# Kernel tuning notes

Hardware: AMD Instinct MI355X
Metric: run time of the kernel (lower is better)

## Reference

```python
import jax, jax.numpy as jnp
import numpy as np

N, C, H, W = 8, 256, 56, 56
DEPTH, HEADS, NWIN, TOPK, MLPR = 4, 8, 7, 4, 4
EPS = 1e-6


def setup_inputs() -> dict:
    key = jax.random.key(0)
    ks = jax.random.split(key, 16)
    s = 0.02
    return {
        'x': jax.random.normal(ks[0], (N, C, H, W), jnp.float32),
        'ln1_w': jnp.ones((DEPTH, C), jnp.float32),
        'ln1_b': jnp.zeros((DEPTH, C), jnp.float32),
        'qkv_w': jax.random.normal(ks[1], (DEPTH, C, 3 * C), jnp.float32) * s,
        'qkv_b': jnp.zeros((DEPTH, 3 * C), jnp.float32),
        'lepe_w': jax.random.normal(ks[2], (DEPTH, C, 1, 5, 5), jnp.float32) * s,
        'lepe_b': jnp.zeros((DEPTH, C), jnp.float32),
        'wo_w': jax.random.normal(ks[3], (DEPTH, C, C), jnp.float32) * s,
        'wo_b': jnp.zeros((DEPTH, C), jnp.float32),
        'ln2_w': jnp.ones((DEPTH, C), jnp.float32),
        'ln2_b': jnp.zeros((DEPTH, C), jnp.float32),
        'mlp1_w': jax.random.normal(ks[4], (DEPTH, C, MLPR * C), jnp.float32) * s,
        'mlp1_b': jnp.zeros((DEPTH, MLPR * C), jnp.float32),
        'mlp2_w': jax.random.normal(ks[5], (DEPTH, MLPR * C, C), jnp.float32) * s,
        'mlp2_b': jnp.zeros((DEPTH, C), jnp.float32),
        'cse1_w': jax.random.normal(ks[6], (C // 16, C), jnp.float32) * s,
        'cse1_b': jnp.zeros((C // 16,), jnp.float32),
        'cse2_w': jax.random.normal(ks[7], (C, C // 16), jnp.float32) * s,
        'cse2_b': jnp.zeros((C,), jnp.float32),
        'sse_w': jax.random.normal(ks[8], (C, C), jnp.float32) * s,
        'sse_b': jnp.zeros((C,), jnp.float32),
        'conv_w': jax.random.normal(ks[9], (C, C, 3, 3), jnp.float32) * s,
        'conv_b': jnp.zeros((C,), jnp.float32),
    }


def _layernorm(x, w, b):
    mu = x.mean(-1, keepdims=True)
    var = ((x - mu) ** 2).mean(-1, keepdims=True)
    return (x - mu) * jax.lax.rsqrt(var + EPS) * w + b


def _dwconv5(x_nchw, k, b):
    # depthwise 5x5 conv, padding 2; k: (C,1,5,5)
    y = jax.lax.conv_general_dilated(
        x_nchw, k, (1, 1), [(2, 2), (2, 2)],
        dimension_numbers=('NCHW', 'OIHW', 'NCHW'), feature_group_count=C)
    return y + b[None, :, None, None]


def _bra(xn, qkv_w, qkv_b, lepe_w, lepe_b, wo_w, wo_b):
    # Bi-level routing attention on NHWC input (already layer-normed).
    j = NWIN; hh = H // j; ww = W // j; p2 = j * j; hw = hh * ww
    scale = C ** -0.5  # qk_dim == dim
    qkv = xn @ qkv_w + qkv_b                      # [N,H,W,3C]
    q, k, v = jnp.split(qkv, 3, axis=-1)

    def to_regions(t):  # [N,H,W,C] -> [N,p2,hw,C]
        return t.reshape(N, j, hh, j, ww, C).transpose(0, 1, 3, 2, 4, 5).reshape(N, p2, hw, C)

    q_pix, k_pix, v_pix = to_regions(q), to_regions(k), to_regions(v)
    # region-level descriptors (routing is detached in original: diff_routing=False)
    q_win = jax.lax.stop_gradient(q_pix.mean(2))  # [N,p2,C]
    k_win = jax.lax.stop_gradient(k_pix.mean(2))
    logits = jnp.einsum('npc,nqc->npq', q_win * scale, k_win)
    _, idx = jax.lax.top_k(logits, TOPK)          # [N,p2,TOPK]; routing weights unused (mul_weight='none')
    bidx = jnp.arange(N)[:, None, None]
    k_sel = k_pix[bidx, idx]                      # [N,p2,TOPK,hw,C] irregular gather
    v_sel = v_pix[bidx, idx]
    m = HEADS; cd = C // m
    qh = q_pix.reshape(N, p2, hw, m, cd)
    kh = k_sel.reshape(N, p2, TOPK * hw, m, cd)
    vh = v_sel.reshape(N, p2, TOPK * hw, m, cd)
    attn = jnp.einsum('npqmc,npkmc->npmqk', qh * scale, kh)
    attn = jax.nn.softmax(attn, axis=-1)
    out = jnp.einsum('npmqk,npkmc->npqmc', attn, vh).reshape(N, p2, hw, C)
    out = out.reshape(N, j, j, hh, ww, C).transpose(0, 1, 3, 2, 4, 5).reshape(N, H, W, C)
    lepe = _dwconv5(v.transpose(0, 3, 1, 2), lepe_w, lepe_b).transpose(0, 2, 3, 1)
    return (out + lepe) @ wo_w + wo_b


def _forward(x, ln1_w, ln1_b, qkv_w, qkv_b, lepe_w, lepe_b, wo_w, wo_b,
             ln2_w, ln2_b, mlp1_w, mlp1_b, mlp2_w, mlp2_b,
             cse1_w, cse1_b, cse2_w, cse2_b, sse_w, sse_b, conv_w, conv_b):
    xh = x.transpose(0, 2, 3, 1)  # NCHW -> NHWC
    for i in range(DEPTH):
        xh = xh + _bra(_layernorm(xh, ln1_w[i], ln1_b[i]),
                       qkv_w[i], qkv_b[i], lepe_w[i], lepe_b[i], wo_w[i], wo_b[i])
        xn = _layernorm(xh, ln2_w[i], ln2_b[i])
        h = jax.nn.gelu(xn @ mlp1_w[i] + mlp1_b[i], approximate=False)
        xh = xh + h @ mlp2_w[i] + mlp2_b[i]
    y = xh.transpose(0, 3, 1, 2)  # NHWC -> NCHW
    # SCSE gating
    pooled = y.mean((2, 3))  # [N,C] adaptive avg pool
    c = jax.nn.relu(pooled @ cse1_w.T + cse1_b)
    c = jax.nn.sigmoid(c @ cse2_w.T + cse2_b)  # [N,C]
    s = jax.nn.sigmoid(jnp.einsum('nchw,oc->nohw', y, sse_w) + sse_b[None, :, None, None])
    y = y * c[:, :, None, None] + y * s
    # final 3x3 conv, padding 1
    y = jax.lax.conv_general_dilated(
        y, conv_w, (1, 1), [(1, 1), (1, 1)],
        dimension_numbers=('NCHW', 'OIHW', 'NCHW')) + conv_b[None, :, None, None]
    return y


def reference(x, ln1_w, ln1_b, qkv_w, qkv_b, lepe_w, lepe_b, wo_w, wo_b,
              ln2_w, ln2_b, mlp1_w, mlp1_b, mlp2_w, mlp2_b,
              cse1_w, cse1_b, cse2_w, cse2_b, sse_w, sse_b, conv_w, conv_b):
    return _forward(x, ln1_w, ln1_b, qkv_w, qkv_b, lepe_w, lepe_b, wo_w, wo_b,
                    ln2_w, ln2_b, mlp1_w, mlp1_b, mlp2_w, mlp2_b,
                    cse1_w, cse1_b, cse2_w, cse2_b, sse_w, sse_b, conv_w, conv_b)
```

## Files before the change

kernel.cpp:

```cpp
#include <hip/hip_runtime.h>

#define PIX 25088
#define NB 8
#define HH 56
#define WW 56
#define CC 256
#define P2 49
#define TOPKN 4

typedef short s16x8 __attribute__((ext_vector_type(8)));
typedef float f32x4 __attribute__((ext_vector_type(4)));

__device__ __forceinline__ float gelu_f(float v){
    return 0.5f*v*(1.0f+erff(v*0.70710678118654752f));
}
__device__ __forceinline__ float sigmoid_f(float v){
    return 1.0f/(1.0f+__expf(-v));
}
__device__ __forceinline__ unsigned short f2bf(float f){
    union { float f; unsigned u; } x; x.f = f;
    unsigned r = x.u + 0x7fffu + ((x.u >> 16) & 1u);
    return (unsigned short)(r >> 16);
}
__device__ __forceinline__ float bf2f(unsigned short u){
    union { unsigned u; float f; } x; x.u = ((unsigned)u) << 16; return x.f;
}
__device__ __forceinline__ void gload_lds16(const void* g, void* l){
    __builtin_amdgcn_global_load_lds((const __attribute__((address_space(1))) void*)g,
                                     (__attribute__((address_space(3))) void*)l, 16, 0, 0);
}

__global__ __launch_bounds__(1024) void nchw_to_nhwc(const float* __restrict__ in, float* __restrict__ out){
    __shared__ float t[32][33];
    int pb = blockIdx.x;
    int n  = pb / 98;
    int p0 = (pb % 98) * 32;
    int c0 = blockIdx.y * 32;
    int tx = threadIdx.x, ty = threadIdx.y;
    t[ty][tx] = in[(size_t)(n*CC + c0+ty)*3136 + p0 + tx];
    __syncthreads();
    out[(size_t)(n*3136 + p0 + ty)*CC + c0 + tx] = t[tx][ty];
}

__global__ __launch_bounds__(1024) void wtrans(const float* __restrict__ in, unsigned short* __restrict__ out,
                                               int K, int N){
    int layer = blockIdx.z;
    in  += (size_t)layer*K*N;
    out += (size_t)layer*K*N;
    __shared__ float t[32][33];
    int n0 = blockIdx.x*32, k0 = blockIdx.y*32;
    t[threadIdx.y][threadIdx.x] = in[(size_t)(k0+threadIdx.y)*N + n0 + threadIdx.x];
    __syncthreads();
    out[(size_t)(n0+threadIdx.y)*K + k0 + threadIdx.x] = f2bf(t[threadIdx.x][threadIdx.y]);
}

__global__ __launch_bounds__(256) void tobf16(const float* __restrict__ in, unsigned short* __restrict__ out, int n){
    int i = blockIdx.x*256 + threadIdx.x;
    if(i < n) out[i] = f2bf(in[i]);
}

__global__ __launch_bounds__(256) void convw_reorder(const float* __restrict__ in, unsigned short* __restrict__ out){
    int idx = blockIdx.x*256 + threadIdx.x;
    if(idx >= 256*256*9) return;
    int o = idx / (256*9); int rem = idx % (256*9); int c = rem/9; int t = rem%9;
    out[(size_t)t*65536 + o*256 + c] = f2bf(in[idx]);
}

__global__ __launch_bounds__(256) void ln_bf16(const float* __restrict__ x, const float* __restrict__ w,
                                               const float* __restrict__ b, unsigned short* __restrict__ y){
    int row = blockIdx.x*4 + (threadIdx.x >> 6);
    int lane = threadIdx.x & 63;
    const float4 v = *reinterpret_cast<const float4*>(&x[(size_t)row*CC + lane*4]);
    float s = v.x + v.y + v.z + v.w;
    #pragma unroll
    for(int off=32; off>0; off>>=1) s += __shfl_xor(s, off);
    float mu = s*(1.0f/CC);
    float d0=v.x-mu, d1=v.y-mu, d2=v.z-mu, d3=v.w-mu;
    float sq = d0*d0 + d1*d1 + d2*d2 + d3*d3;
    #pragma unroll
    for(int off=32; off>0; off>>=1) sq += __shfl_xor(sq, off);
    float rs = rsqrtf(sq*(1.0f/CC) + 1e-6f);
    const float4 wv = *reinterpret_cast<const float4*>(&w[lane*4]);
    const float4 bv = *reinterpret_cast<const float4*>(&b[lane*4]);
    ushort4 o;
    o.x = f2bf(d0*rs*wv.x + bv.x);
    o.y = f2bf(d1*rs*wv.y + bv.y);
    o.z = f2bf(d2*rs*wv.z + bv.z);
    o.w = f2bf(d3*rs*wv.w + bv.w);
    *reinterpret_cast<ushort4*>(&y[(size_t)row*CC + lane*4]) = o;
}

template<int EPI, bool HASRES, bool OUTF, bool OUTB>
__global__ __launch_bounds__(256) void mfma_gemm(
    const unsigned short* __restrict__ A, const unsigned short* __restrict__ Bt,
    const float* __restrict__ bias, const float* __restrict__ res,
    const float* __restrict__ gfac,
    float* __restrict__ Cf, unsigned short* __restrict__ Cb,
    int M, int N, int K)
{
    __shared__ __align__(16) unsigned short As[4096];
    __shared__ __align__(16) unsigned short Bs[4096];
    const int tid = threadIdx.x;
    const int wid = tid >> 6, lane = tid & 63;
    const int row0 = blockIdx.y << 7, col0 = blockIdx.x << 7;
    const int wm = wid >> 1, wn = wid & 1;
    const int li = lane & 15, qq = lane >> 4;

    f32x4 acc[4][4] = {};
    const int nk = K >> 5;
    for(int kt=0; kt<nk; kt++){
        const int k0 = kt << 5;
        #pragma unroll
        for(int i=0;i<2;i++){
            int boff = wid*2048 + i*1024 + (lane<<4);
            int row = boff >> 6;
            int t = (boff >> 4) & 3;
            int q = t ^ ((row >> 1) & 3);
            gload_lds16(A  + (size_t)(row0+row)*K + k0 + q*8, (char*)As + wid*2048 + i*1024);
            gload_lds16(Bt + (size_t)(col0+row)*K + k0 + q*8, (char*)Bs + wid*2048 + i*1024);
        }
        __syncthreads();
        s16x8 af[4], bfr[4];
        #pragma unroll
        for(int mi=0;mi<4;mi++){
            int r = (wm<<6) + (mi<<4) + li;
            af[mi] = *(const s16x8*)((const char*)As + r*64 + ((qq ^ ((r>>1)&3))<<4));
        }
        #pragma unroll
        for(int nj=0;nj<4;nj++){
            int r = (wn<<6) + (nj<<4) + li;
            bfr[nj] = *(const s16x8*)((const char*)Bs + r*64 + ((qq ^ ((r>>1)&3))<<4));
        }
        #pragma unroll
        for(int mi=0;mi<4;mi++)
            #pragma unroll
            for(int nj=0;nj<4;nj++)
                acc[mi][nj] = __builtin_amdgcn_mfma_f32_16x16x32_bf16(af[mi], bfr[nj], acc[mi][nj], 0,0,0);
        __syncthreads();
    }
    #pragma unroll
    for(int mi=0;mi<4;mi++){
        #pragma unroll
        for(int nj=0;nj<4;nj++){
            int col = col0 + (wn<<6) + (nj<<4) + li;
            float bv = bias ? bias[col] : 0.0f;
            #pragma unroll
            for(int rr=0;rr<4;rr++){
                int row = row0 + (wm<<6) + (mi<<4) + (qq<<2) + rr;
                float v = acc[mi][nj][rr] + bv;
                if(EPI==1) v = gelu_f(v);
                if(EPI==2) v = sigmoid_f(v);
                if(EPI==3){
                    int n = row / 3136; int rem = row % 3136;
                    int h = rem / 56, w = rem % 56;
                    float xv = res[(size_t)row*N + col];
                    v = xv*(gfac[n*CC + col] + sigmoid_f(v));
                    size_t dst = ((size_t)(64 + n*3364 + (h+1)*58 + (w+1)))*CC + col;
                    Cb[dst] = f2bf(v);
                } else {
                    if(HASRES) v += res[(size_t)row*N + col];
                    if(OUTF) Cf[(size_t)row*N + col] = v;
                    if(OUTB) Cb[(size_t)row*N + col] = f2bf(v);
                }
            }
        }
    }
}

__global__ __launch_bounds__(256) void conv_gemm(
    const unsigned short* __restrict__ P, const unsigned short* __restrict__ CBt,
    const float* __restrict__ bias, float* __restrict__ out)
{
    __shared__ __align__(16) unsigned short As[4096];
    __shared__ __align__(16) unsigned short Bs[4096];
    const int tid = threadIdx.x;
    const int wid = tid >> 6, lane = tid & 63;
    const int row0 = blockIdx.y << 7, col0 = blockIdx.x << 7;
    const int wm = wid >> 1, wn = wid & 1;
    const int li = lane & 15, qq = lane >> 4;
    const int K = 256;

    f32x4 acc[4][4] = {};
    for(int tap=0; tap<9; tap++){
        int d = ((tap/3)-1)*58 + (tap%3) - 1;
        const unsigned short* A  = P + (size_t)(64 + d)*256;
        const unsigned short* Bt = CBt + (size_t)tap*65536;
        for(int kt=0; kt<8; kt++){
            const int k0 = kt << 5;
            #pragma unroll
            for(int i=0;i<2;i++){
                int boff = wid*2048 + i*1024 + (lane<<4);
                int row = boff >> 6;
                int t = (boff >> 4) & 3;
                int q = t ^ ((row >> 1) & 3);
                gload_lds16(A  + (size_t)(row0+row)*K + k0 + q*8, (char*)As + wid*2048 + i*1024);
                gload_lds16(Bt + (size_t)(col0+row)*K + k0 + q*8, (char*)Bs + wid*2048 + i*1024);
            }
            __syncthreads();
            s16x8 af[4], bfr[4];
            #pragma unroll
            for(int mi=0;mi<4;mi++){
                int r = (wm<<6) + (mi<<4) + li;
                af[mi] = *(const s16x8*)((const char*)As + r*64 + ((qq ^ ((r>>1)&3))<<4));
            }
            #pragma unroll
            for(int nj=0;nj<4;nj++){
                int r = (wn<<6) + (nj<<4) + li;
                bfr[nj] = *(const s16x8*)((const char*)Bs + r*64 + ((qq ^ ((r>>1)&3))<<4));
            }
            #pragma unroll
            for(int mi=0;mi<4;mi++)
                #pragma unroll
                for(int nj=0;nj<4;nj++)
                    acc[mi][nj] = __builtin_amdgcn_mfma_f32_16x16x32_bf16(af[mi], bfr[nj], acc[mi][nj], 0,0,0);
            __syncthreads();
        }
    }
    #pragma unroll
    for(int mi=0;mi<4;mi++){
        #pragma unroll
        for(int nj=0;nj<4;nj++){
            int col = col0 + (wn<<6) + (nj<<4) + li;
            float bv = bias[col];
            #pragma unroll
            for(int rr=0;rr<4;rr++){
                int prow = row0 + (wm<<6) + (mi<<4) + (qq<<2) + rr;
                if(prow < NB*3364){
                    int n = prow / 3364; int rem = prow % 3364;
                    int y = rem / 58, x = rem % 58;
                    if(y>=1 && y<57 && x>=1 && x<57){
                        out[(((size_t)n*CC + col)*HH + (y-1))*WW + (x-1)] = acc[mi][nj][rr] + bv;
                    }
                }
            }
        }
    }
}

__global__ __launch_bounds__(256) void winmean_kernel(const unsigned short* __restrict__ qkv,
                                                      float* __restrict__ qwin, float* __restrict__ kwin){
    int b = blockIdx.x;
    int n = b / P2, p = b % P2;
    int c = threadIdx.x;
    int hb = (p/7)*8, wb = (p%7)*8;
    float sq=0.f, sk=0.f;
    for(int pixi=0;pixi<64;pixi++){
        int h = hb + (pixi>>3), w = wb + (pixi&7);
        const unsigned short* row = &qkv[((size_t)(n*HH+h)*WW + w)*768];
        sq += bf2f(row[c]);
        sk += bf2f(row[256+c]);
    }
    qwin[(size_t)b*CC+c] = sq*(1.0f/64.0f);
    kwin[(size_t)b*CC+c] = sk*(1.0f/64.0f);
}

__global__ __launch_bounds__(64) void route_kernel(const float* __restrict__ qwin, const float* __restrict__ kwin,
                                                   int* __restrict__ idxout){
    int b = blockIdx.x;
    int n = b / P2;
    int j = threadIdx.x;
    __shared__ float lg[64];
    float v = -1e30f;
    if(j < P2){
        const float* q = &qwin[(size_t)b*CC];
        const float* k = &kwin[(size_t)(n*P2+j)*CC];
        float s=0.f;
        for(int c=0;c<CC;c++) s += q[c]*k[c];
        v = s*0.0625f;
    }
    lg[j] = v;
    __syncthreads();
    if(j==0){
        for(int t=0;t<TOPKN;t++){
            int best=0; float bv=lg[0];
            for(int u=1;u<P2;u++) if(lg[u]>bv){bv=lg[u];best=u;}
            idxout[b*TOPKN+t]=best;
            lg[best]=-1e30f;
        }
    }
}

__global__ __launch_bounds__(64) void attn_kernel(const unsigned short* __restrict__ qkv,
                                                  const int* __restrict__ idx,
                                                  float* __restrict__ out){
    __shared__ __align__(16) unsigned short P_lds[64*32];
    __shared__ int pixo[256];
    int b = blockIdx.x;
    int m = b & 7; int np = b >> 3;
    int n = np / P2, p = np % P2;
    int lane = threadIdx.x;
    int li = lane & 15, g = lane >> 4;
    int hb = (p/7)*8, wb = (p%7)*8;

    #pragma unroll
    for(int t4=0;t4<4;t4++){
        int r = idx[np*TOPKN + t4];
        int pixi = lane;
        int h = (r/7)*8 + (pixi>>3), w = (r%7)*8 + (pixi&7);
        pixo[t4*64 + lane] = (n*HH+h)*WW + w;
    }
    __syncthreads();

    s16x8 qfr[4];
    #pragma unroll
    for(int q4=0;q4<4;q4++){
        int q = q4*16 + li;
        int h = hb + (q>>3), w = wb + (q&7);
        qfr[q4] = *reinterpret_cast<const s16x8*>(&qkv[((size_t)(n*HH+h)*WW + w)*768 + m*32 + g*8]);
    }

    const float SC = 0.0625f * 1.44269504088896f;
    f32x4 ot[2][4] = {};
    float mx[4], lsum[4];
    #pragma unroll
    for(int q4=0;q4<4;q4++){ mx[q4] = -3e38f; lsum[q4] = 0.0f; }

    for(int kb=0; kb<8; kb++){
        f32x4 st[2][4] = {};
        #pragma unroll
        for(int kf=0;kf<2;kf++){
            int key = kb*32 + kf*16 + li;
            s16x8 kfrag = *reinterpret_cast<const s16x8*>(&qkv[(size_t)pixo[key]*768 + 256 + m*32 + g*8]);
            #pragma unroll
            for(int q4=0;q4<4;q4++)
                st[kf][q4] = __builtin_amdgcn_mfma_f32_16x16x32_bf16(kfrag, qfr[q4], st[kf][q4], 0,0,0);
        }
        #pragma unroll
        for(int kf=0;kf<2;kf++)
            #pragma unroll
            for(int q4=0;q4<4;q4++)
                #pragma unroll
                for(int r=0;r<4;r++) st[kf][q4][r] *= SC;
        #pragma unroll
        for(int q4=0;q4<4;q4++){
            float pm = st[0][q4][0];
            #pragma unroll
            for(int r=1;r<4;r++) pm = fmaxf(pm, st[0][q4][r]);
            #pragma unroll
            for(int r=0;r<4;r++) pm = fmaxf(pm, st[1][q4][r]);
            pm = fmaxf(pm, __shfl_xor(pm, 16));
            pm = fmaxf(pm, __shfl_xor(pm, 32));
            float mnew = fmaxf(mx[q4], pm);
            float fsc = exp2f(mx[q4] - mnew);
            mx[q4] = mnew;
            float ps = 0.0f;
            #pragma unroll
            for(int kf=0;kf<2;kf++)
                #pragma unroll
                for(int r=0;r<4;r++){
                    float pv = exp2f(st[kf][q4][r] - mnew);
                    st[kf][q4][r] = pv;
                    ps += pv;
                }
            ps += __shfl_xor(ps, 16);
            ps += __shfl_xor(ps, 32);
            lsum[q4] = lsum[q4]*fsc + ps;
            #pragma unroll
            for(int chf=0;chf<2;chf++)
                #pragma unroll
                for(int r=0;r<4;r++) ot[chf][q4][r] *= fsc;
        }
        #pragma unroll
        for(int q4=0;q4<4;q4++){
            int q = q4*16 + li;
            #pragma unroll
            for(int kf=0;kf<2;kf++){
                unsigned lo = ((unsigned)f2bf(st[kf][q4][0])) | (((unsigned)f2bf(st[kf][q4][1]))<<16);
                unsigned hi = ((unsigned)f2bf(st[kf][q4][2])) | (((unsigned)f2bf(st[kf][q4][3]))<<16);
                int byte = (q*64 + kf*32 + g*8) ^ ((q&3)<<4);
                *reinterpret_cast<uint2*>((char*)P_lds + byte) = make_uint2(lo, hi);
            }
        }
        __syncthreads();
        s16x8 pfr[4];
        #pragma unroll
        for(int q4=0;q4<4;q4++){
            int q = q4*16 + li;
            int byte = (q*64 + g*16) ^ ((q&3)<<4);
            pfr[q4] = *reinterpret_cast<const s16x8*>((const char*)P_lds + byte);
        }
        #pragma unroll
        for(int chf=0;chf<2;chf++){
            s16x8 vfr;
            #pragma unroll
            for(int j=0;j<8;j++){
                int key = kb*32 + g*8 + j;
                vfr[j] = (short)qkv[(size_t)pixo[key]*768 + 512 + m*32 + chf*16 + li];
            }
            #pragma unroll
            for(int q4=0;q4<4;q4++)
                ot[chf][q4] = __builtin_amdgcn_mfma_f32_16x16x32_bf16(vfr, pfr[q4], ot[chf][q4], 0,0,0);
        }
        __syncthreads();
    }
    #pragma unroll
    for(int q4=0;q4<4;q4++){
        int q = q4*16 + li;
        int h = hb + (q>>3), w = wb + (q&7);
        float inv = 1.0f / lsum[q4];
        float* orow = &out[((size_t)(n*HH+h)*WW + w)*CC + m*32];
        #pragma unroll
        for(int chf=0;chf<2;chf++)
            #pragma unroll
            for(int r=0;r<4;r++)
                orow[chf*16 + g*4 + r] = ot[chf][q4][r]*inv;
    }
}

__global__ __launch_bounds__(256) void lepe_kernel(const unsigned short* __restrict__ qkv,
                                                   const float* __restrict__ attn,
                                                   const float* __restrict__ lw, const float* __restrict__ lb,
                                                   unsigned short* __restrict__ outb){
    __shared__ float tile[144][64];
    int tileid = blockIdx.x;
    int cg = blockIdx.y;
    int n = blockIdx.z;
    int hb = (tileid/7)*8, wb = (tileid%7)*8;
    int tid = threadIdx.x;
    for(int ii=tid; ii<144*64; ii+=256){
        int sp = ii >> 6, cl = ii & 63;
        int ty = sp / 12, tx = sp % 12;
        int y = hb + ty - 2, x = wb + tx - 2;
        float v = 0.0f;
        if(y>=0 && y<HH && x>=0 && x<WW)
            v = bf2f(qkv[((size_t)(n*HH+y)*WW + x)*768 + 512 + cg*64 + cl]);
        tile[sp][cl] = v;
    }
    __syncthreads();
    int cl = tid & 63;
    int c = cg*64 + cl;
    float wv[25];
    #pragma unroll
    for(int t=0;t<25;t++) wv[t] = lw[c*25 + t];
    float bias = lb[c];
    for(int oi = tid; oi < 4096; oi += 256){
        int sp = oi >> 6;
        int py = sp >> 3, px = sp & 7;
        float a = bias;
        #pragma unroll
        for(int dy=0;dy<5;dy++)
            #pragma unroll
            for(int dx=0;dx<5;dx++)
                a += tile[(py+dy)*12 + px+dx][cl]*wv[dy*5+dx];
        size_t pix = (size_t)(n*HH + hb+py)*WW + wb+px;
        outb[pix*CC + c] = f2bf(attn[pix*CC + c] + a);
    }
}

__global__ __launch_bounds__(256) void pool_kernel(const float* __restrict__ x, float* __restrict__ pooled){
    int n = blockIdx.y, c = threadIdx.x;
    int p0 = blockIdx.x*64;
    float s=0.f;
    for(int pp=0;pp<64;pp++) s += x[((size_t)n*3136 + p0 + pp)*CC + c];
    atomicAdd(&pooled[n*CC+c], s*(1.0f/3136.0f));
}

__global__ __launch_bounds__(256) void cse_kernel(const float* __restrict__ pooled,
                                                  const float* __restrict__ w1, const float* __restrict__ b1,
                                                  const float* __restrict__ w2, const float* __restrict__ b2,
                                                  float* __restrict__ cfac){
    int n = blockIdx.x, t = threadIdx.x;
    __shared__ float c1[16];
    if(t < 16){
        float s = b1[t];
        for(int c=0;c<CC;c++) s += pooled[n*CC+c]*w1[t*CC+c];
        c1[t] = fmaxf(s, 0.0f);
    }
    __syncthreads();
    float s = b2[t];
    #pragma unroll
    for(int j=0;j<16;j++) s += c1[j]*w2[t*16+j];
    cfac[n*CC+t] = sigmoid_f(s);
}

extern "C" void kernel_launch(void* const* d_in, const int* in_sizes, int n_in,
                              void* d_out, int out_size, void* d_ws, size_t ws_size,
                              hipStream_t stream){
    const float* x_in   = (const float*)d_in[0];
    const float* ln1w   = (const float*)d_in[1];
    const float* ln1b   = (const float*)d_in[2];
    const float* qkvw   = (const float*)d_in[3];
    const float* qkvb   = (const float*)d_in[4];
    const float* lepew  = (const float*)d_in[5];
    const float* lepeb  = (const float*)d_in[6];
    const float* wow    = (const float*)d_in[7];
    const float* wob    = (const float*)d_in[8];
    const float* ln2w   = (const float*)d_in[9];
    const float* ln2b   = (const float*)d_in[10];
    const float* mlp1w  = (const float*)d_in[11];
    const float* mlp1b  = (const float*)d_in[12];
    const float* mlp2w  = (const float*)d_in[13];
    const float* mlp2b  = (const float*)d_in[14];
    const float* cse1w  = (const float*)d_in[15];
    const float* cse1b  = (const float*)d_in[16];
    const float* cse2w  = (const float*)d_in[17];
    const float* cse2b  = (const float*)d_in[18];
    const float* ssew   = (const float*)d_in[19];
    const float* sseb   = (const float*)d_in[20];
    const float* convw  = (const float*)d_in[21];
    const float* convb  = (const float*)d_in[22];
    float* out = (float*)d_out;

    char* base = (char*)d_ws;
    float* bufx   = (float*)base;                         base += (size_t)PIX*CC*4;
    float* buftmp = (float*)base;                         base += (size_t)PIX*CC*4;
    unsigned short* qkvB = (unsigned short*)base;
    unsigned short* hid  = (unsigned short*)base;
    unsigned short* Ppad = (unsigned short*)base;         base += (size_t)PIX*1024*2;
    float* qwin   = (float*)base;                         base += (size_t)NB*P2*CC*4;
    float* kwin   = (float*)base;                         base += (size_t)NB*P2*CC*4;
    float* pooled = (float*)base;                         base += NB*CC*4;
    float* cfac   = (float*)base;                         base += NB*CC*4;
    int*   idxb   = (int*)base;                           base += 2048*4;
    unsigned short* bufxn = (unsigned short*)base;        base += (size_t)PIX*CC*2;
    unsigned short* qkvbt = (unsigned short*)base;        base += (size_t)4*768*256*2;
    unsigned short* wobt  = (unsigned short*)base;        base += (size_t)4*256*256*2;
    unsigned short* m1bt  = (unsigned short*)base;        base += (size_t)4*1024*256*2;
    unsigned short* m2bt  = (unsigned short*)base;        base += (size_t)4*256*1024*2;
    unsigned short* ssebt = (unsigned short*)base;        base += (size_t)256*256*2;
    unsigned short* cvbt  = (unsigned short*)base;        base += (size_t)9*256*256*2;

    wtrans<<<dim3(24, 8, 4), dim3(32,32), 0, stream>>>(qkvw, qkvbt, 256, 768);
    wtrans<<<dim3(8, 8, 4),  dim3(32,32), 0, stream>>>(wow,  wobt,  256, 256);
    wtrans<<<dim3(32, 8, 4), dim3(32,32), 0, stream>>>(mlp1w, m1bt, 256, 1024);
    wtrans<<<dim3(8, 32, 4), dim3(32,32), 0, stream>>>(mlp2w, m2bt, 1024, 256);
    tobf16<<<256, 256, 0, stream>>>(ssew, ssebt, 65536);
    convw_reorder<<<2304, 256, 0, stream>>>(convw, cvbt);

    nchw_to_nhwc<<<dim3(NB*98, 8), dim3(32,32), 0, stream>>>(x_in, bufx);

    for(int i=0;i<4;i++){
        ln_bf16<<<PIX/4,256,0,stream>>>(bufx, ln1w+i*CC, ln1b+i*CC, bufxn);
        mfma_gemm<0,false,false,true><<<dim3(6,196),256,0,stream>>>(
            bufxn, qkvbt+(size_t)i*768*256, qkvb+i*768, nullptr, nullptr, nullptr, qkvB, PIX, 768, 256);
        winmean_kernel<<<NB*P2,256,0,stream>>>(qkvB, qwin, kwin);
        route_kernel<<<NB*P2,64,0,stream>>>(qwin, kwin, idxb);
        attn_kernel<<<NB*P2*8,64,0,stream>>>(qkvB, idxb, buftmp);
        lepe_kernel<<<dim3(49,4,NB),256,0,stream>>>(qkvB, buftmp, lepew+(size_t)i*CC*25, lepeb+i*CC, bufxn);
        mfma_gemm<0,true,true,false><<<dim3(2,196),256,0,stream>>>(
            bufxn, wobt+(size_t)i*256*256, wob+i*CC, bufx, nullptr, bufx, nullptr, PIX, 256, 256);
        ln_bf16<<<PIX/4,256,0,stream>>>(bufx, ln2w+i*CC, ln2b+i*CC, bufxn);
        mfma_gemm<1,false,false,true><<<dim3(8,196),256,0,stream>>>(
            bufxn, m1bt+(size_t)i*1024*256, mlp1b+i*1024, nullptr, nullptr, nullptr, hid, PIX, 1024, 256);
        mfma_gemm<0,true,true,false><<<dim3(2,196),256,0,stream>>>(
            hid, m2bt+(size_t)i*256*1024, mlp2b+i*CC, bufx, nullptr, bufx, nullptr, PIX, 256, 1024);
    }

    hipMemsetAsync(pooled, 0, NB*CC*sizeof(float), stream);
    pool_kernel<<<dim3(49,NB),256,0,stream>>>(bufx, pooled);
    cse_kernel<<<NB,256,0,stream>>>(pooled, cse1w, cse1b, cse2w, cse2b, cfac);
    tobf16<<<PIX,256,0,stream>>>(bufx, bufxn, PIX*CC);
    hipMemsetAsync(Ppad, 0, (size_t)27136*256*2, stream);
    mfma_gemm<3,false,false,false><<<dim3(2,196),256,0,stream>>>(
        bufxn, ssebt, sseb, bufx, cfac, nullptr, Ppad, PIX, 256, 256);
    conv_gemm<<<dim3(2,211),256,0,stream>>>(Ppad, cvbt, convb, out);
}
```

Baseline: 1.283 ms.

## Double GEMM K-tile to 64 with new swizzle; store attention output as bf16

The shared MFMA GEMM and the implicit-GEMM conv kernel now stage 64-wide K slices in LDS, using a new 8-slot XOR swizzle. This halves the number of barrier pairs per K loop and doubles the LDS footprint per block, which may reduce occupancy. Separately, the attention kernel now writes its output in bf16 rather than fp32, and the LePE kernel reads it back as bf16. That halves the traffic of that intermediate buffer at the cost of slightly lower precision.

```diff
diff --git a/kernel.cpp b/kernel.cpp
--- a/kernel.cpp
+++ b/kernel.cpp
@@ -98,44 +98,48 @@
     float* __restrict__ Cf, unsigned short* __restrict__ Cb,
     int M, int N, int K)
 {
-    __shared__ __align__(16) unsigned short As[4096];
-    __shared__ __align__(16) unsigned short Bs[4096];
+    __shared__ __align__(16) unsigned short As[8192];
+    __shared__ __align__(16) unsigned short Bs[8192];
     const int tid = threadIdx.x;
     const int wid = tid >> 6, lane = tid & 63;
     const int row0 = blockIdx.y << 7, col0 = blockIdx.x << 7;
     const int wm = wid >> 1, wn = wid & 1;
     const int li = lane & 15, qq = lane >> 4;
+    const int grow = (wid<<5) + (lane>>3);
+    const int gq   = (lane&7) ^ ((lane>>3)&7);
 
     f32x4 acc[4][4] = {};
-    const int nk = K >> 5;
+    const int nk = K >> 6;
     for(int kt=0; kt<nk; kt++){
-        const int k0 = kt << 5;
-        #pragma unroll
-        for(int i=0;i<2;i++){
-            int boff = wid*2048 + i*1024 + (lane<<4);
-            int row = boff >> 6;
-            int t = (boff >> 4) & 3;
-            int q = t ^ ((row >> 1) & 3);
-            gload_lds16(A  + (size_t)(row0+row)*K + k0 + q*8, (char*)As + wid*2048 + i*1024);
-            gload_lds16(Bt + (size_t)(col0+row)*K + k0 + q*8, (char*)Bs + wid*2048 + i*1024);
+        const int k0 = kt << 6;
+        #pragma unroll
+        for(int i=0;i<4;i++){
+            int r = grow + i*8;
+            gload_lds16(A  + (size_t)(row0+r)*K + k0 + gq*8, (char*)As + wid*4096 + i*1024);
+            gload_lds16(Bt + (size_t)(col0+r)*K + k0 + gq*8, (char*)Bs + wid*4096 + i*1024);
         }
         __syncthreads();
-        s16x8 af[4], bfr[4];
-        #pragma unroll
-        for(int mi=0;mi<4;mi++){
-            int r = (wm<<6) + (mi<<4) + li;
-            af[mi] = *(const s16x8*)((const char*)As + r*64 + ((qq ^ ((r>>1)&3))<<4));
-        }
-        #pragma unroll
-        for(int nj=0;nj<4;nj++){
-            int r = (wn<<6) + (nj<<4) + li;
-            bfr[nj] = *(const s16x8*)((const char*)Bs + r*64 + ((qq ^ ((r>>1)&3))<<4));
-        }
-        #pragma unroll
-        for(int mi=0;mi<4;mi++)
-            #pragma unroll
-            for(int nj=0;nj<4;nj++)
-                acc[mi][nj] = __builtin_amdgcn_mfma_f32_16x16x32_bf16(af[mi], bfr[nj], acc[mi][nj], 0,0,0);
+        #pragma unroll
+        for(int ks=0;ks<2;ks++){
+            s16x8 af[4], bfr[4];
+            #pragma unroll
+            for(int mi=0;mi<4;mi++){
+                int r = (wm<<6) + (mi<<4) + li;
+                int slot = (ks*4+qq) ^ (r&7);
+                af[mi] = *(const s16x8*)((const char*)As + r*128 + slot*16);
+            }
+            #pragma unroll
+            for(int nj=0;nj<4;nj++){
+                int r = (wn<<6) + (nj<<4) + li;
+                int slot = (ks*4+qq) ^ (r&7);
+                bfr[nj] = *(const s16x8*)((const char*)Bs + r*128 + slot*16);
+            }
+            #pragma unroll
+            for(int mi=0;mi<4;mi++)
+                #pragma unroll
+                for(int nj=0;nj<4;nj++)
+                    acc[mi][nj] = __builtin_amdgcn_mfma_f32_16x16x32_bf16(af[mi], bfr[nj], acc[mi][nj], 0,0,0);
+        }
         __syncthreads();
     }
     #pragma unroll
@@ -171,13 +175,15 @@
     const unsigned short* __restrict__ P, const unsigned short* __restrict__ CBt,
     const float* __restrict__ bias, float* __restrict__ out)
 {
-    __shared__ __align__(16) unsigned short As[4096];
-    __shared__ __align__(16) unsigned short Bs[4096];
+    __shared__ __align__(16) unsigned short As[8192];
+    __shared__ __align__(16) unsigned short Bs[8192];
     const int tid = threadIdx.x;
     const int wid = tid >> 6, lane = tid & 63;
     const int row0 = blockIdx.y << 7, col0 = blockIdx.x << 7;
     const int wm = wid >> 1, wn = wid & 1;
     const int li = lane & 15, qq = lane >> 4;
+    const int grow = (wid<<5) + (lane>>3);
+    const int gq   = (lane&7) ^ ((lane>>3)&7);
     const int K = 256;
 
     f32x4 acc[4][4] = {};
@@ -185,34 +191,36 @@
         int d = ((tap/3)-1)*58 + (tap%3) - 1;
         const unsigned short* A  = P + (size_t)(64 + d)*256;
         const unsigned short* Bt = CBt + (size_t)tap*65536;
-        for(int kt=0; kt<8; kt++){
-            const int k0 = kt << 5;
-            #pragma unroll
-            for(int i=0;i<2;i++){
-                int boff = wid*2048 + i*1024 + (lane<<4);
-                int row = boff >> 6;
-                int t = (boff >> 4) & 3;
-                int q = t ^ ((row >> 1) & 3);
-                gload_lds16(A  + (size_t)(row0+row)*K + k0 + q*8, (char*)As + wid*2048 + i*1024);
-                gload_lds16(Bt + (size_t)(col0+row)*K + k0 + q*8, (char*)Bs + wid*2048 + i*1024);
+        for(int kt=0; kt<4; kt++){
+            const int k0 = kt << 6;
+            #pragma unroll
+            for(int i=0;i<4;i++){
+                int r = grow + i*8;
+                gload_lds16(A  + (size_t)(row0+r)*K + k0 + gq*8, (char*)As + wid*4096 + i*1024);
+                gload_lds16(Bt + (size_t)(col0+r)*K + k0 + gq*8, (char*)Bs + wid*4096 + i*1024);
             }
             __syncthreads();
-            s16x8 af[4], bfr[4];
-            #pragma unroll
-            for(int mi=0;mi<4;mi++){
-                int r = (wm<<6) + (mi<<4) + li;
-                af[mi] = *(const s16x8*)((const char*)As + r*64 + ((qq ^ ((r>>1)&3))<<4));
-            }
-            #pragma unroll
-            for(int nj=0;nj<4;nj++){
-                int r = (wn<<6) + (nj<<4) + li;
-                bfr[nj] = *(const s16x8*)((const char*)Bs + r*64 + ((qq ^ ((r>>1)&3))<<4));
-            }
-            #pragma unroll
-            for(int mi=0;mi<4;mi++)
-                #pragma unroll
-                for(int nj=0;nj<4;nj++)
-                    acc[mi][nj] = __builtin_amdgcn_mfma_f32_16x16x32_bf16(af[mi], bfr[nj], acc[mi][nj], 0,0,0);
+            #pragma unroll
+            for(int ks=0;ks<2;ks++){
+                s16x8 af[4], bfr[4];
+                #pragma unroll
+                for(int mi=0;mi<4;mi++){
+                    int r = (wm<<6) + (mi<<4) + li;
+                    int slot = (ks*4+qq) ^ (r&7);
+                    af[mi] = *(const s16x8*)((const char*)As + r*128 + slot*16);
+                }
+                #pragma unroll
+                for(int nj=0;nj<4;nj++){
+                    int r = (wn<<6) + (nj<<4) + li;
+                    int slot = (ks*4+qq) ^ (r&7);
+                    bfr[nj] = *(const s16x8*)((const char*)Bs + r*128 + slot*16);
+                }
+                #pragma unroll
+                for(int mi=0;mi<4;mi++)
+                    #pragma unroll
+                    for(int nj=0;nj<4;nj++)
+                        acc[mi][nj] = __builtin_amdgcn_mfma_f32_16x16x32_bf16(af[mi], bfr[nj], acc[mi][nj], 0,0,0);
+            }
             __syncthreads();
         }
     }
@@ -282,7 +290,7 @@
 
 __global__ __launch_bounds__(64) void attn_kernel(const unsigned short* __restrict__ qkv,
                                                   const int* __restrict__ idx,
-                                                  float* __restrict__ out){
+                                                  unsigned short* __restrict__ out){
     __shared__ __align__(16) unsigned short P_lds[64*32];
     __shared__ int pixo[256];
     int b = blockIdx.x;
@@ -398,17 +406,17 @@
         int q = q4*16 + li;
         int h = hb + (q>>3), w = wb + (q&7);
         float inv = 1.0f / lsum[q4];
-        float* orow = &out[((size_t)(n*HH+h)*WW + w)*CC + m*32];
+        unsigned short* orow = &out[((size_t)(n*HH+h)*WW + w)*CC + m*32];
         #pragma unroll
         for(int chf=0;chf<2;chf++)
             #pragma unroll
             for(int r=0;r<4;r++)
-                orow[chf*16 + g*4 + r] = ot[chf][q4][r]*inv;
+                orow[chf*16 + g*4 + r] = f2bf(ot[chf][q4][r]*inv);
     }
 }
 
 __global__ __launch_bounds__(256) void lepe_kernel(const unsigned short* __restrict__ qkv,
-                                                   const float* __restrict__ attn,
+                                                   const unsigned short* __restrict__ attn,
                                                    const float* __restrict__ lw, const float* __restrict__ lb,
                                                    unsigned short* __restrict__ outb){
     __shared__ float tile[144][64];
@@ -443,7 +451,7 @@
             for(int dx=0;dx<5;dx++)
                 a += tile[(py+dy)*12 + px+dx][cl]*wv[dy*5+dx];
         size_t pix = (size_t)(n*HH + hb+py)*WW + wb+px;
-        outb[pix*CC + c] = f2bf(attn[pix*CC + c] + a);
+        outb[pix*CC + c] = f2bf(bf2f(attn[pix*CC + c]) + a);
     }
 }
 
@@ -520,6 +528,8 @@
     unsigned short* ssebt = (unsigned short*)base;        base += (size_t)256*256*2;
     unsigned short* cvbt  = (unsigned short*)base;        base += (size_t)9*256*256*2;
 
+    unsigned short* attnB = (unsigned short*)buftmp;
+
     wtrans<<<dim3(24, 8, 4), dim3(32,32), 0, stream>>>(qkvw, qkvbt, 256, 768);
     wtrans<<<dim3(8, 8, 4),  dim3(32,32), 0, stream>>>(wow,  wobt,  256, 256);
     wtrans<<<dim3(32, 8, 4), dim3(32,32), 0, stream>>>(mlp1w, m1bt, 256, 1024);
@@ -535,8 +545,8 @@
             bufxn, qkvbt+(size_t)i*768*256, qkvb+i*768, nullptr, nullptr, nullptr, qkvB, PIX, 768, 256);
         winmean_kernel<<<NB*P2,256,0,stream>>>(qkvB, qwin, kwin);
         route_kernel<<<NB*P2,64,0,stream>>>(qwin, kwin, idxb);
-        attn_kernel<<<NB*P2*8,64,0,stream>>>(qkvB, idxb, buftmp);
-        lepe_kernel<<<dim3(49,4,NB),256,0,stream>>>(qkvB, buftmp, lepew+(size_t)i*CC*25, lepeb+i*CC, bufxn);
+        attn_kernel<<<NB*P2*8,64,0,stream>>>(qkvB, idxb, attnB);
+        lepe_kernel<<<dim3(49,4,NB),256,0,stream>>>(qkvB, attnB, lepew+(size_t)i*CC*25, lepeb+i*CC, bufxn);
         mfma_gemm<0,true,true,false><<<dim3(2,196),256,0,stream>>>(
             bufxn, wobt+(size_t)i*256*256, wob+i*CC, bufx, nullptr, bufx, nullptr, PIX, 256, 256);
         ln_bf16<<<PIX/4,256,0,stream>>>(bufx, ln2w+i*CC, ln2b+i*CC, bufxn);
```

Measured after the change: 1.343 ms. 1.05x slower.
